# Performance work log

Hardware: AMD Instinct MI355X
Metric: run time of the kernel (lower is better)

Reference implementation:

```python
import jax, jax.numpy as jnp
import numpy as np

B = 256
DIM_IN = 1024
DIM_GLOBAL = 1024
U = 512          # num_units = sum(num_units_regions)
D = 16           # dim_attention_unit
G = 8            # num_attention_groups
NEG_INF = -jnp.inf


def setup_inputs() -> dict:
    key = jax.random.key(0)
    ks = jax.random.split(key, 8)
    x = jax.random.normal(ks[0], (B, DIM_IN), dtype=jnp.float32)
    # learned params (xavier-ish scale)
    W1 = jax.random.normal(ks[1], (DIM_IN, DIM_GLOBAL), dtype=jnp.float32) * (1.0 / np.sqrt(DIM_IN))
    b1 = jnp.zeros((DIM_GLOBAL,), dtype=jnp.float32)
    W2 = jax.random.normal(ks[2], (DIM_GLOBAL, U * D), dtype=jnp.float32) * (1.0 / np.sqrt(DIM_GLOBAL))
    b2 = jnp.zeros((U * D,), dtype=jnp.float32)
    temperature = jnp.ones((U,), dtype=jnp.float32)
    mem_attention = jax.random.normal(ks[3], (B, U, D), dtype=jnp.float32)
    mem_value = jax.random.normal(ks[4], (B, U, D), dtype=jnp.float32)
    return {"x": x, "W1": W1, "b1": b1, "W2": W2, "b2": b2,
            "temperature": temperature,
            "mem_attention": mem_attention, "mem_value": mem_value}


def reference(x, W1, b1, W2, b2, temperature, mem_attention, mem_value):
    batch = x.shape[0]
    # two-layer linear projection -> per-unit attention keys [B, U, D]
    h = x @ W1 + b1
    attention = (h @ W2 + b2).reshape(batch, U, D)
    # broadcast mul-sum score over d: [B, M, U]  (M == batch)
    weights = jnp.einsum('bud,mud->bmu', attention, mem_attention)
    weights = weights * temperature  # per-unit temperature, broadcasts over last axis
    # mask_p = 0.0 -> random mask is a no-op (per original code's early return)
    # eye mask: query i cannot attend to memory slot i
    eye = jnp.eye(batch, dtype=bool)[:, :, None]
    weights = jnp.where(eye, NEG_INF, weights)
    # grouped softmax over the memory axis within each group of size batch // G
    w = weights.reshape(batch, batch // G, G, U)
    w = jax.nn.softmax(w, axis=1)
    weights = w.reshape(batch, batch, U) / 8.0
    # weighted sum over memory slots: [B, U, D]
    outputs = jnp.einsum('bmu,mud->bud', weights, mem_value)
    return (attention, weights, outputs)
```

## Files before the change

### kernel.cpp

```cpp
#include <hip/hip_runtime.h>
#include <hip/hip_bf16.h>
#include <math.h>

#define Bq 256
#define DIM_IN 1024
#define DIM_GLOBAL 1024
#define UNITS 512
#define DD 16
#define GG 8
#define ATT_ELEMS (256*512*16)
#define W_ELEMS   (256*256*512)
#define SCRATCH_BYTES ((size_t)512*256*256*4)

typedef __attribute__((ext_vector_type(8))) short bf16x8;
typedef __attribute__((ext_vector_type(4))) float f32x4;

__device__ __forceinline__ short f2bf(float f) {
    union { float f; unsigned u; } v; v.f = f;
    unsigned u = v.u;
    u += 0x7fffu + ((u >> 16) & 1u);
    return (short)(u >> 16);
}

__device__ __forceinline__ unsigned pk2(float a, float b) {
    return (unsigned)(unsigned short)f2bf(a) | ((unsigned)(unsigned short)f2bf(b) << 16);
}

#define BK 32
#define ASTR 40
#define BSTR 40

__global__ __launch_bounds__(256) void gemm_bias(
    const float* __restrict__ A, const float* __restrict__ B,
    const float* __restrict__ bias, float* __restrict__ C,
    int M, int N, int K)
{
    __shared__ __align__(16) short As[64 * ASTR];
    __shared__ __align__(16) short Bs[64 * BSTR];

    const int t = threadIdx.x;
    const int lane = t & 63;
    const int wave = t >> 6;
    const int m0 = blockIdx.y * 64;
    const int n0 = blockIdx.x * 64;

    const int wm = (wave >> 1) * 32;
    const int wn = (wave & 1) * 32;
    const int fl = lane & 15;
    const int ko = lane >> 4;

    f32x4 acc00 = {}, acc01 = {}, acc10 = {}, acc11 = {};

    const int ar = t >> 2;
    const int aq = (t & 3) * 8;
    const int bn = t & 63;
    const int bk = (t >> 6) * 8;

    for (int k0 = 0; k0 < K; k0 += BK) {
        __syncthreads();
        {
            const float* src = A + (m0 + ar) * K + k0 + aq;
            float4 v0 = *(const float4*)(src);
            float4 v1 = *(const float4*)(src + 4);
            bf16x8 p;
            p[0]=f2bf(v0.x); p[1]=f2bf(v0.y); p[2]=f2bf(v0.z); p[3]=f2bf(v0.w);
            p[4]=f2bf(v1.x); p[5]=f2bf(v1.y); p[6]=f2bf(v1.z); p[7]=f2bf(v1.w);
            *(bf16x8*)(&As[ar * ASTR + aq]) = p;
        }
        {
            const float* src = B + (k0 + bk) * N + n0 + bn;
            bf16x8 p;
            #pragma unroll
            for (int j = 0; j < 8; j++) p[j] = f2bf(src[j * N]);
            *(bf16x8*)(&Bs[bn * BSTR + bk]) = p;
        }
        __syncthreads();

        bf16x8 a0 = *(const bf16x8*)(&As[(wm + 0  + fl) * ASTR + ko * 8]);
        bf16x8 a1 = *(const bf16x8*)(&As[(wm + 16 + fl) * ASTR + ko * 8]);
        bf16x8 b0 = *(const bf16x8*)(&Bs[(wn + 0  + fl) * BSTR + ko * 8]);
        bf16x8 b1 = *(const bf16x8*)(&Bs[(wn + 16 + fl) * BSTR + ko * 8]);
        acc00 = __builtin_amdgcn_mfma_f32_16x16x32_bf16(a0, b0, acc00, 0, 0, 0);
        acc01 = __builtin_amdgcn_mfma_f32_16x16x32_bf16(a0, b1, acc01, 0, 0, 0);
        acc10 = __builtin_amdgcn_mfma_f32_16x16x32_bf16(a1, b0, acc10, 0, 0, 0);
        acc11 = __builtin_amdgcn_mfma_f32_16x16x32_bf16(a1, b1, acc11, 0, 0, 0);
    }

    #pragma unroll
    for (int r = 0; r < 4; r++) {
        int mrow = m0 + wm + ko * 4 + r;
        int ncol = n0 + wn + fl;
        C[(mrow     ) * N + (ncol     )] = acc00[r] + bias[ncol];
        C[(mrow     ) * N + (ncol + 16)] = acc01[r] + bias[ncol + 16];
        C[(mrow + 16) * N + (ncol     )] = acc10[r] + bias[ncol];
        C[(mrow + 16) * N + (ncol + 16)] = acc11[r] + bias[ncol + 16];
    }
}

#define L2E 1.4426950408889634f

__global__ __launch_bounds__(256) void attn_mfma(
    const float* __restrict__ attention,
    const float* __restrict__ mem_att,
    const float* __restrict__ mem_val,
    const float* __restrict__ temperature,
    float* __restrict__ scratch,
    float* __restrict__ outputs_out)
{
    const int t    = threadIdx.x;
    const int lane = t & 63;
    const int lq   = lane >> 4;
    const int lr   = lane & 15;
    const int W    = blockIdx.x * 4 + (t >> 6);
    const int u    = W >> 3;
    const int btp  = W & 7;
    const bool ldq = (lq < 2);

    const float tl2e = temperature[u] * L2E;
    const f32x4 zf = {0.f, 0.f, 0.f, 0.f};

    bf16x8 kf[16];
    #pragma unroll
    for (int mt = 0; mt < 16; mt++) {
        bf16x8 p = {0,0,0,0,0,0,0,0};
        if (ldq) {
            const float* src = mem_att + (size_t)(mt*16 + lr) * 8192 + u * 16 + lq * 8;
            float4 v0 = *(const float4*)(src);
            float4 v1 = *(const float4*)(src + 4);
            p[0]=f2bf(v0.x); p[1]=f2bf(v0.y); p[2]=f2bf(v0.z); p[3]=f2bf(v0.w);
            p[4]=f2bf(v1.x); p[5]=f2bf(v1.y); p[6]=f2bf(v1.z); p[7]=f2bf(v1.w);
        }
        kf[mt] = p;
    }
    bf16x8 af[2];
    #pragma unroll
    for (int bb = 0; bb < 2; bb++) {
        bf16x8 p = {0,0,0,0,0,0,0,0};
        if (ldq) {
            const int bt = btp * 2 + bb;
            const float* src = attention + (size_t)(bt*16 + lr) * 8192 + u * 16 + lq * 8;
            float4 v0 = *(const float4*)(src);
            float4 v1 = *(const float4*)(src + 4);
            p[0]=f2bf(v0.x); p[1]=f2bf(v0.y); p[2]=f2bf(v0.z); p[3]=f2bf(v0.w);
            p[4]=f2bf(v1.x); p[5]=f2bf(v1.y); p[6]=f2bf(v1.z); p[7]=f2bf(v1.w);
        }
        af[bb] = p;
    }

    f32x4 gacc[2] = {zf, zf};
    #pragma unroll
    for (int mt = 0; mt < 16; mt++) {
        #pragma unroll
        for (int bb = 0; bb < 2; bb++) {
            f32x4 s = __builtin_amdgcn_mfma_f32_16x16x32_bf16(kf[mt], af[bb], zf, 0, 0, 0);
            const int bg = (btp*2 + bb)*16 + lr;
            #pragma unroll
            for (int r = 0; r < 4; r++) {
                const int m = mt*16 + lq*4 + r;
                const float e = (m == bg) ? 0.f : exp2f(s[r] * tl2e);
                gacc[bb][r] += e;
            }
        }
    }
    f32x4 rinv[2];
    #pragma unroll
    for (int bb = 0; bb < 2; bb++)
        #pragma unroll
        for (int r = 0; r < 4; r++) {
            const float tot = gacc[bb][r] + __shfl_xor(gacc[bb][r], 32);
            rinv[bb][r] = 1.0f / (8.0f * tot);
        }

    f32x4 oacc[2] = {zf, zf};
    auto load_vfrag = [&](int mt) -> bf16x8 {
        bf16x8 p = {0,0,0,0,0,0,0,0};
        if (ldq) {
            const float* base = mem_val + (size_t)(mt*16 + lq*8) * 8192 + u * 16 + lr;
            #pragma unroll
            for (int j = 0; j < 8; j++) p[j] = f2bf(base[(size_t)j * 8192]);
        }
        return p;
    };
    bf16x8 vf_n = load_vfrag(0);
    #pragma unroll
    for (int mt = 0; mt < 16; mt++) {
        const bf16x8 vf = vf_n;
        if (mt < 15) vf_n = load_vfrag(mt + 1);
        #pragma unroll
        for (int bb = 0; bb < 2; bb++) {
            f32x4 s = __builtin_amdgcn_mfma_f32_16x16x32_bf16(kf[mt], af[bb], zf, 0, 0, 0);
            const int bg = (btp*2 + bb)*16 + lr;
            float w4[4];
            #pragma unroll
            for (int r = 0; r < 4; r++) {
                const int m = mt*16 + lq*4 + r;
                const float e = (m == bg) ? 0.f : exp2f(s[r] * tl2e);
                w4[r] = e * rinv[bb][r];
            }
            float* sp = scratch + (size_t)u * 65536 + (size_t)(mt*16 + lq*4) * 256 + bg;
            #pragma unroll
            for (int r = 0; r < 4; r++) sp[(size_t)r * 256] = w4[r];
            const unsigned d0 = pk2(w4[0], w4[1]);
            const unsigned d1 = pk2(w4[2], w4[3]);
            const unsigned x0 = (unsigned)__shfl_xor((int)d0, 16);
            const unsigned x1 = (unsigned)__shfl_xor((int)d1, 16);
            const unsigned y0 = (unsigned)__shfl_xor((int)d0, 32);
            const unsigned y1 = (unsigned)__shfl_xor((int)d1, 32);
            const unsigned z0 = (unsigned)__shfl_xor((int)d0, 48);
            const unsigned z1 = (unsigned)__shfl_xor((int)d1, 48);
            union { unsigned uu[4]; bf16x8 v; } wf;
            if (lq == 0)      { wf.uu[0]=d0; wf.uu[1]=d1; wf.uu[2]=x0; wf.uu[3]=x1; }
            else if (lq == 1) { wf.uu[0]=z0; wf.uu[1]=z1; wf.uu[2]=y0; wf.uu[3]=y1; }
            else              { wf.uu[0]=0;  wf.uu[1]=0;  wf.uu[2]=0;  wf.uu[3]=0;  }
            oacc[bb] = __builtin_amdgcn_mfma_f32_16x16x32_bf16(wf.v, vf, oacc[bb], 0, 0, 0);
        }
    }

    #pragma unroll
    for (int bb = 0; bb < 2; bb++) {
        #pragma unroll
        for (int r = 0; r < 4; r++) {
            const int bg = (btp*2 + bb)*16 + lq*4 + r;
            outputs_out[(size_t)bg * 8192 + u * 16 + lr] = oacc[bb][r];
        }
    }
}

__global__ __launch_bounds__(256) void w_transpose(
    const float* __restrict__ scr, float* __restrict__ wout)
{
    const int t    = threadIdx.x;
    const int lane = t & 63;
    const int bx   = blockIdx.x;
    const int m    = bx & 255;
    const int u0   = ((bx >> 8) & 7) << 6;
    const int bt16 = (bx >> 11) * 4 + (t >> 6);
    const int U    = u0 + 4 * (lane & 15);
    const int B    = bt16 * 16 + 4 * (lane >> 4);

    float4 ld[4];
    #pragma unroll
    for (int i = 0; i < 4; i++)
        ld[i] = *(const float4*)(scr + ((size_t)(U + i) << 16) + (m << 8) + B);
    #pragma unroll
    for (int j = 0; j < 4; j++) {
        float4 v;
        v.x = ld[0][j]; v.y = ld[1][j]; v.z = ld[2][j]; v.w = ld[3][j];
        *(float4*)(wout + ((size_t)(B + j) << 17) + (m << 9) + U) = v;
    }
}

__global__ __launch_bounds__(256) void attn_fused_fb(
    const float* __restrict__ attention,
    const float* __restrict__ mem_att,
    const float* __restrict__ mem_val,
    const float* __restrict__ temperature,
    float* __restrict__ weights_out,
    float* __restrict__ outputs_out)
{
    const int t = threadIdx.x;
    const int ublk = blockIdx.x & 15;
    const int bblk = blockIdx.x >> 4;
    const int u  = ublk * 32 + (t & 31);
    const int b  = bblk * 8 + (t >> 5);

    float att[16];
    {
        const float* ap = attention + (size_t)(b * UNITS + u) * DD;
        #pragma unroll
        for (int d4 = 0; d4 < 4; d4++) {
            float4 v = *(const float4*)(ap + d4 * 4);
            att[d4*4+0]=v.x; att[d4*4+1]=v.y; att[d4*4+2]=v.z; att[d4*4+3]=v.w;
        }
    }
    const float tl2e = temperature[u] * L2E;
    const float* kbase = mem_att + u * DD;

    float gsum[8];
    #pragma unroll
    for (int g = 0; g < 8; g++) gsum[g] = 0.f;

    for (int m8 = 0; m8 < 256; m8 += 8) {
        #pragma unroll
        for (int g = 0; g < 8; g++) {
            const int m = m8 + g;
            const float* kp = kbase + m * (UNITS * DD);
            float s = 0.f;
            #pragma unroll
            for (int d4 = 0; d4 < 4; d4++) {
                float4 v = *(const float4*)(kp + d4 * 4);
                s += att[d4*4+0]*v.x + att[d4*4+1]*v.y
                   + att[d4*4+2]*v.z + att[d4*4+3]*v.w;
            }
            const float e = (m == b) ? 0.f : exp2f(s * tl2e);
            gsum[g] += e;
        }
    }
    float rinv[8];
    #pragma unroll
    for (int g = 0; g < 8; g++) rinv[g] = 1.0f / (8.0f * gsum[g]);

    float acc[16];
    #pragma unroll
    for (int d = 0; d < 16; d++) acc[d] = 0.f;
    const float* vbase = mem_val + u * DD;
    float* wrow = weights_out + (size_t)b * (256 * UNITS) + u;

    for (int m8 = 0; m8 < 256; m8 += 8) {
        #pragma unroll
        for (int g = 0; g < 8; g++) {
            const int m = m8 + g;
            const float* kp = kbase + m * (UNITS * DD);
            float s = 0.f;
            #pragma unroll
            for (int d4 = 0; d4 < 4; d4++) {
                float4 v = *(const float4*)(kp + d4 * 4);
                s += att[d4*4+0]*v.x + att[d4*4+1]*v.y
                   + att[d4*4+2]*v.z + att[d4*4+3]*v.w;
            }
            const float e = (m == b) ? 0.f : exp2f(s * tl2e);
            const float w = e * rinv[g];
            wrow[(size_t)m * UNITS] = w;
            const float* vp = vbase + m * (UNITS * DD);
            #pragma unroll
            for (int d4 = 0; d4 < 4; d4++) {
                float4 v = *(const float4*)(vp + d4 * 4);
                acc[d4*4+0] += w * v.x; acc[d4*4+1] += w * v.y;
                acc[d4*4+2] += w * v.z; acc[d4*4+3] += w * v.w;
            }
        }
    }
    float* op = outputs_out + (size_t)(b * UNITS + u) * DD;
    #pragma unroll
    for (int d4 = 0; d4 < 4; d4++) {
        float4 v;
        v.x = acc[d4*4+0]; v.y = acc[d4*4+1];
        v.z = acc[d4*4+2]; v.w = acc[d4*4+3];
        *(float4*)(op + d4 * 4) = v;
    }
}

extern "C" void kernel_launch(void* const* d_in, const int* in_sizes, int n_in,
                              void* d_out, int out_size, void* d_ws, size_t ws_size,
                              hipStream_t stream) {
    const float* x        = (const float*)d_in[0];
    const float* W1       = (const float*)d_in[1];
    const float* b1       = (const float*)d_in[2];
    const float* W2       = (const float*)d_in[3];
    const float* b2       = (const float*)d_in[4];
    const float* temp     = (const float*)d_in[5];
    const float* mem_att  = (const float*)d_in[6];
    const float* mem_val  = (const float*)d_in[7];

    float* out       = (float*)d_out;
    float* attention = out;
    float* weights   = out + ATT_ELEMS;
    float* outputs   = out + ATT_ELEMS + W_ELEMS;

    float* h = weights;

    dim3 blk(256);
    gemm_bias<<<dim3(DIM_GLOBAL / 64, Bq / 64), blk, 0, stream>>>(
        x, W1, b1, h, Bq, DIM_GLOBAL, DIM_IN);
    gemm_bias<<<dim3((UNITS * DD) / 64, Bq / 64), blk, 0, stream>>>(
        h, W2, b2, attention, Bq, UNITS * DD, DIM_GLOBAL);

    if (ws_size >= SCRATCH_BYTES && d_ws != nullptr) {
        float* scratch = (float*)d_ws;
        attn_mfma<<<dim3(1024), blk, 0, stream>>>(
            attention, mem_att, mem_val, temp, scratch, outputs);
        w_transpose<<<dim3(8192), blk, 0, stream>>>(scratch, weights);
    } else {
        attn_fused_fb<<<dim3(512), blk, 0, stream>>>(
            attention, mem_att, mem_val, temp, weights, outputs);
    }
}
```

Baseline: 370.9 us.

## One batch tile per wave, shuffle-free MFMA operand layout, swizzled block order

Each wave now handles a single 16-row batch tile instead of two, and the grid is doubled to 2048 blocks, giving more parallelism and fewer registers per wave. The second MFMA's K dimension is remapped so each lane pairs two consecutive 16-row memory tiles, which removes the cross-lane shuffles used to assemble the weight operand. All lanes now load value fragments and the loop processes two m-tiles per iteration. Block indices are swizzled so that consecutive blocks touch different units. The cost is redundant loading of the mem_attention fragments across twice as many waves.

```diff
diff --git a/kernel.cpp b/kernel.cpp
--- a/kernel.cpp
+++ b/kernel.cpp
@@ -111,13 +111,16 @@
     const int lane = t & 63;
     const int lq   = lane >> 4;
     const int lr   = lane & 15;
-    const int W    = blockIdx.x * 4 + (t >> 6);
-    const int u    = W >> 3;
-    const int btp  = W & 7;
+    const int bid  = blockIdx.x;
+    const int swz  = (bid & 7) * 256 + (bid >> 3);
+    const int W    = swz * 4 + (t >> 6);
+    const int u    = W >> 4;
+    const int bt   = W & 15;
     const bool ldq = (lq < 2);
 
     const float tl2e = temperature[u] * L2E;
     const f32x4 zf = {0.f, 0.f, 0.f, 0.f};
+    const int bg = bt * 16 + lr;
 
     bf16x8 kf[16];
     #pragma unroll
@@ -132,97 +135,83 @@
         }
         kf[mt] = p;
     }
-    bf16x8 af[2];
-    #pragma unroll
-    for (int bb = 0; bb < 2; bb++) {
-        bf16x8 p = {0,0,0,0,0,0,0,0};
-        if (ldq) {
-            const int bt = btp * 2 + bb;
-            const float* src = attention + (size_t)(bt*16 + lr) * 8192 + u * 16 + lq * 8;
-            float4 v0 = *(const float4*)(src);
-            float4 v1 = *(const float4*)(src + 4);
-            p[0]=f2bf(v0.x); p[1]=f2bf(v0.y); p[2]=f2bf(v0.z); p[3]=f2bf(v0.w);
-            p[4]=f2bf(v1.x); p[5]=f2bf(v1.y); p[6]=f2bf(v1.z); p[7]=f2bf(v1.w);
-        }
-        af[bb] = p;
-    }
-
-    f32x4 gacc[2] = {zf, zf};
+    bf16x8 af = {0,0,0,0,0,0,0,0};
+    if (ldq) {
+        const float* src = attention + (size_t)bg * 8192 + u * 16 + lq * 8;
+        float4 v0 = *(const float4*)(src);
+        float4 v1 = *(const float4*)(src + 4);
+        af[0]=f2bf(v0.x); af[1]=f2bf(v0.y); af[2]=f2bf(v0.z); af[3]=f2bf(v0.w);
+        af[4]=f2bf(v1.x); af[5]=f2bf(v1.y); af[6]=f2bf(v1.z); af[7]=f2bf(v1.w);
+    }
+
+    f32x4 gacc = zf;
     #pragma unroll
     for (int mt = 0; mt < 16; mt++) {
-        #pragma unroll
-        for (int bb = 0; bb < 2; bb++) {
-            f32x4 s = __builtin_amdgcn_mfma_f32_16x16x32_bf16(kf[mt], af[bb], zf, 0, 0, 0);
-            const int bg = (btp*2 + bb)*16 + lr;
-            #pragma unroll
-            for (int r = 0; r < 4; r++) {
-                const int m = mt*16 + lq*4 + r;
-                const float e = (m == bg) ? 0.f : exp2f(s[r] * tl2e);
-                gacc[bb][r] += e;
-            }
-        }
-    }
-    f32x4 rinv[2];
-    #pragma unroll
-    for (int bb = 0; bb < 2; bb++)
+        f32x4 s = __builtin_amdgcn_mfma_f32_16x16x32_bf16(kf[mt], af, zf, 0, 0, 0);
         #pragma unroll
         for (int r = 0; r < 4; r++) {
-            const float tot = gacc[bb][r] + __shfl_xor(gacc[bb][r], 32);
-            rinv[bb][r] = 1.0f / (8.0f * tot);
-        }
-
-    f32x4 oacc[2] = {zf, zf};
-    auto load_vfrag = [&](int mt) -> bf16x8 {
-        bf16x8 p = {0,0,0,0,0,0,0,0};
-        if (ldq) {
-            const float* base = mem_val + (size_t)(mt*16 + lq*8) * 8192 + u * 16 + lr;
-            #pragma unroll
-            for (int j = 0; j < 8; j++) p[j] = f2bf(base[(size_t)j * 8192]);
-        }
-        return p;
+            const int m = mt*16 + lq*4 + r;
+            gacc[r] += (m == bg) ? 0.f : exp2f(s[r] * tl2e);
+        }
+    }
+    f32x4 rinv;
+    #pragma unroll
+    for (int r = 0; r < 4; r++) {
+        const float tot = gacc[r] + __shfl_xor(gacc[r], 32);
+        rinv[r] = 1.0f / (8.0f * tot);
+    }
+
+    auto load_vpair = [&](int p) -> bf16x8 {
+        const float* base = mem_val + (size_t)(p*32 + lq*4) * 8192 + u * 16 + lr;
+        bf16x8 vv;
+        #pragma unroll
+        for (int j = 0; j < 4; j++) {
+            vv[j]     = f2bf(base[(size_t)j * 8192]);
+            vv[4 + j] = f2bf(base[(size_t)(16 + j) * 8192]);
+        }
+        return vv;
     };
-    bf16x8 vf_n = load_vfrag(0);
-    #pragma unroll
-    for (int mt = 0; mt < 16; mt++) {
-        const bf16x8 vf = vf_n;
-        if (mt < 15) vf_n = load_vfrag(mt + 1);
-        #pragma unroll
-        for (int bb = 0; bb < 2; bb++) {
-            f32x4 s = __builtin_amdgcn_mfma_f32_16x16x32_bf16(kf[mt], af[bb], zf, 0, 0, 0);
-            const int bg = (btp*2 + bb)*16 + lr;
-            float w4[4];
-            #pragma unroll
-            for (int r = 0; r < 4; r++) {
-                const int m = mt*16 + lq*4 + r;
-                const float e = (m == bg) ? 0.f : exp2f(s[r] * tl2e);
-                w4[r] = e * rinv[bb][r];
-            }
-            float* sp = scratch + (size_t)u * 65536 + (size_t)(mt*16 + lq*4) * 256 + bg;
-            #pragma unroll
-            for (int r = 0; r < 4; r++) sp[(size_t)r * 256] = w4[r];
-            const unsigned d0 = pk2(w4[0], w4[1]);
-            const unsigned d1 = pk2(w4[2], w4[3]);
-            const unsigned x0 = (unsigned)__shfl_xor((int)d0, 16);
-            const unsigned x1 = (unsigned)__shfl_xor((int)d1, 16);
-            const unsigned y0 = (unsigned)__shfl_xor((int)d0, 32);
-            const unsigned y1 = (unsigned)__shfl_xor((int)d1, 32);
-            const unsigned z0 = (unsigned)__shfl_xor((int)d0, 48);
-            const unsigned z1 = (unsigned)__shfl_xor((int)d1, 48);
-            union { unsigned uu[4]; bf16x8 v; } wf;
-            if (lq == 0)      { wf.uu[0]=d0; wf.uu[1]=d1; wf.uu[2]=x0; wf.uu[3]=x1; }
-            else if (lq == 1) { wf.uu[0]=z0; wf.uu[1]=z1; wf.uu[2]=y0; wf.uu[3]=y1; }
-            else              { wf.uu[0]=0;  wf.uu[1]=0;  wf.uu[2]=0;  wf.uu[3]=0;  }
-            oacc[bb] = __builtin_amdgcn_mfma_f32_16x16x32_bf16(wf.v, vf, oacc[bb], 0, 0, 0);
-        }
-    }
-
-    #pragma unroll
-    for (int bb = 0; bb < 2; bb++) {
+
+    f32x4 oacc = zf;
+    bf16x8 vf = load_vpair(0);
+    float* sbase = scratch + (size_t)u * 65536 + bg;
+
+    #pragma unroll
+    for (int p2 = 0; p2 < 8; p2++) {
+        const bf16x8 vcur = vf;
+        if (p2 < 7) vf = load_vpair(p2 + 1);
+
+        f32x4 sX = __builtin_amdgcn_mfma_f32_16x16x32_bf16(kf[2*p2    ], af, zf, 0, 0, 0);
+        f32x4 sY = __builtin_amdgcn_mfma_f32_16x16x32_bf16(kf[2*p2 + 1], af, zf, 0, 0, 0);
+
+        float wX[4], wY[4];
         #pragma unroll
         for (int r = 0; r < 4; r++) {
-            const int bg = (btp*2 + bb)*16 + lq*4 + r;
-            outputs_out[(size_t)bg * 8192 + u * 16 + lr] = oacc[bb][r];
-        }
+            const int mX = p2*32 + lq*4 + r;
+            const int mY = mX + 16;
+            wX[r] = (mX == bg) ? 0.f : exp2f(sX[r] * tl2e) * rinv[r];
+            wY[r] = (mY == bg) ? 0.f : exp2f(sY[r] * tl2e) * rinv[r];
+        }
+
+        float* spX = sbase + (size_t)(p2*32 + lq*4) * 256;
+        #pragma unroll
+        for (int r = 0; r < 4; r++) spX[(size_t)r * 256] = wX[r];
+        float* spY = spX + 16 * 256;
+        #pragma unroll
+        for (int r = 0; r < 4; r++) spY[(size_t)r * 256] = wY[r];
+
+        union { unsigned uu[4]; bf16x8 v; } wf;
+        wf.uu[0] = pk2(wX[0], wX[1]);
+        wf.uu[1] = pk2(wX[2], wX[3]);
+        wf.uu[2] = pk2(wY[0], wY[1]);
+        wf.uu[3] = pk2(wY[2], wY[3]);
+        oacc = __builtin_amdgcn_mfma_f32_16x16x32_bf16(wf.v, vcur, oacc, 0, 0, 0);
+    }
+
+    #pragma unroll
+    for (int r = 0; r < 4; r++) {
+        const int bo = bt*16 + lq*4 + r;
+        outputs_out[(size_t)bo * 8192 + u * 16 + lr] = oacc[r];
     }
 }
 
@@ -367,7 +356,7 @@
 
     if (ws_size >= SCRATCH_BYTES && d_ws != nullptr) {
         float* scratch = (float*)d_ws;
-        attn_mfma<<<dim3(1024), blk, 0, stream>>>(
+        attn_mfma<<<dim3(2048), blk, 0, stream>>>(
             attention, mem_att, mem_val, temp, scratch, outputs);
         w_transpose<<<dim3(8192), blk, 0, stream>>>(scratch, weights);
     } else {
```

Result: faster. 362.1 us (-2.4%).
